# Kernel optimization log

Measured on AMD Instinct MI355X. Metric: run time of the kernel, lower is better.

The kernel has to match this reference:

```python
import jax, jax.numpy as jnp
import numpy as np

B, N, HID = 2, 512, 768
BIAF = 256
CLS = 14
CH = 32
SIZE_DIM = 25
N_POS = 30
HSZ = 2 * (BIAF + 1) + SIZE_DIM


def setup_inputs() -> dict:
    key = jax.random.key(0)
    ks = jax.random.split(key, 16)
    s = 0.02
    return {
        "x": jax.random.normal(ks[0], (B, N, HID), jnp.float32),
        "y": jax.random.normal(ks[1], (B, N, HID), jnp.float32),
        "z": jax.random.normal(ks[2], (B, N, N, CH), jnp.float32),
        "mlp1_w": jax.random.normal(ks[3], (BIAF, HID), jnp.float32) * s,
        "mlp1_b": jnp.zeros((BIAF,), jnp.float32),
        "mlp2_w": jax.random.normal(ks[4], (BIAF, HID), jnp.float32) * s,
        "mlp2_b": jnp.zeros((BIAF,), jnp.float32),
        "head_w": jax.random.normal(ks[5], (BIAF, HID), jnp.float32) * s,
        "head_b": jnp.zeros((BIAF,), jnp.float32),
        "tail_w": jax.random.normal(ks[6], (BIAF, HID), jnp.float32) * s,
        "tail_b": jnp.zeros((BIAF,), jnp.float32),
        "biaf_W": jax.random.normal(ks[7], (CLS, BIAF + 1, BIAF + 1), jnp.float32) * s,
        "W": jax.random.normal(ks[8], (CLS, HSZ), jnp.float32) * s,
        "size_emb": jax.random.normal(ks[9], (N_POS, SIZE_DIM), jnp.float32) * s,
    }


def reference(x, y, z, mlp1_w, mlp1_b, mlp2_w, mlp2_b, head_w, head_b,
              tail_w, tail_b, biaf_W, W, size_emb):
    # MLP branches (dropout=0 at eval; torch GELU is exact erf)
    h = jax.nn.gelu(x @ mlp1_w.T + mlp1_b, approximate=False)   # (b,m,BIAF)
    t = jax.nn.gelu(y @ mlp2_w.T + mlp2_b, approximate=False)   # (b,n,BIAF)
    ones = jnp.ones(h.shape[:-1] + (1,), h.dtype)
    h1 = jnp.concatenate([h, ones], -1)                          # (b,m,BIAF+1)
    t1 = jnp.concatenate([t, ones], -1)                          # (b,n,BIAF+1)
    # Biaffine with bias_x=bias_y=True -> (b,cls,m,n)
    o1 = jnp.einsum('bmi,kij,bnj->bkmn', h1, biaf_W, t1)

    # head/tail MLPs with LeakyReLU(0.01), then append 1-column
    head = jax.nn.leaky_relu(x @ head_w.T + head_b, 0.01)
    tail = jax.nn.leaky_relu(x @ tail_w.T + tail_b, 0.01)
    head = jnp.concatenate([head, ones], -1)                     # (b,m,BIAF+1)
    tail = jnp.concatenate([tail, ones], -1)                     # (b,n,BIAF+1)

    # einsum('bmnh,kh->bkmn', cat([head_m, tail_n, size_mn]), W) decomposed so
    # the (b,m,n,HSZ) pairwise tensor is never materialized (same math).
    d = head.shape[-1]
    Wh, Wt, Ws = W[:, :d], W[:, d:2 * d], W[:, 2 * d:]
    n = x.shape[1]
    ar = jnp.arange(n)
    ids = jnp.clip(ar[None, :] - ar[:, None], -N_POS // 2, N_POS // 2 - 1) + N_POS // 2
    se = size_emb[ids]                                           # (m,n,SIZE_DIM)
    o3 = (jnp.einsum('bmh,kh->bkm', head, Wh)[:, :, :, None]
          + jnp.einsum('bnh,kh->bkn', tail, Wt)[:, :, None, :]
          + jnp.einsum('mnh,kh->kmn', se, Ws)[None])
    return o1 + o3
```

## Files before the change

kernel.cpp:

```cpp
#include <hip/hip_runtime.h>
#include <hip/hip_bf16.h>
#include <math.h>
#include <stdint.h>

#define BDIM 2
#define NDIM 512
#define HID 768
#define BIAF 256
#define CLS 14
#define DD 257
#define NPOS 30
#define SDIM 25
#define HSZ 539
#define PK 288
#define PJ 384
#define ASTRIDE 296

typedef unsigned short ushort_t;
typedef __attribute__((ext_vector_type(8))) short short8;
typedef __attribute__((ext_vector_type(4))) float floatx4;
typedef __attribute__((ext_vector_type(4))) unsigned short ushort4_t;

#define MFMA16(a, b, c) __builtin_amdgcn_mfma_f32_16x16x32_bf16((a), (b), (c), 0, 0, 0)

__device__ inline float bf2f(ushort_t u) {
    union { unsigned int i; float f; } c; c.i = ((unsigned)u) << 16; return c.f;
}
__device__ inline ushort_t f2bf(float f) {
    __hip_bfloat16 h = __float2bfloat16(f);
    return *(ushort_t*)&h;
}

__device__ inline int xcd_swz(int bid, int nwg) {
    int q = nwg >> 3;
    return (bid & 7) * q + (bid >> 3);
}

__device__ inline void glds16(const ushort_t* g, const ushort_t* l) {
    __builtin_amdgcn_global_load_lds(
        (const __attribute__((address_space(1))) unsigned int*)(unsigned long long)(uintptr_t)g,
        (__attribute__((address_space(3))) unsigned int*)(unsigned int)(uintptr_t)l,
        16, 0, 0);
}


__global__ __launch_bounds__(256) void prep_all(
    const float* __restrict__ biafW, ushort_t* __restrict__ packW,
    const float* __restrict__ x, const float* __restrict__ y,
    const float* __restrict__ m1w, const float* __restrict__ m2w,
    const float* __restrict__ hw,  const float* __restrict__ tw,
    ushort_t* __restrict__ xhi, ushort_t* __restrict__ xlo,
    ushort_t* __restrict__ yhi, ushort_t* __restrict__ ylo,
    ushort_t* __restrict__ whi, ushort_t* __restrict__ wlo,
    ushort_t* __restrict__ h1hi, ushort_t* __restrict__ h1lo,
    ushort_t* __restrict__ t1hi, ushort_t* __restrict__ t1lo)
{
    const int bid = blockIdx.x;
    if (bid < 1512) {
        __shared__ float tile[32][33];
        const int ix = bid % 9;
        const int jy = (bid / 9) % 12;
        const int k  = bid / 108;
        const int i0 = ix * 32, j0 = jy * 32;
        const int r8 = threadIdx.x >> 5;
        const int c  = threadIdx.x & 31;
        #pragma unroll
        for (int rr = 0; rr < 4; ++rr) {
            int r = rr * 8 + r8;
            int gi = i0 + r, gj = j0 + c;
            tile[r][c] = (gi < DD && gj < DD) ? biafW[((size_t)k * DD + gi) * DD + gj] : 0.f;
        }
        __syncthreads();
        #pragma unroll
        for (int rr = 0; rr < 4; ++rr) {
            int jr = rr * 8 + r8;
            packW[((size_t)k * PJ + (j0 + jr)) * PK + i0 + c] = f2bf(tile[c][jr]);
        }
        return;
    }
    int tg = (bid - 1512) * 256 + threadIdx.x;
    if (tg < 196608) {
        int mat = tg / 49152;
        int e0  = (tg % 49152) * 4;
        const float* src = (mat == 0) ? m1w : (mat == 1) ? m2w : (mat == 2) ? hw : tw;
        float4 v = *(const float4*)(src + e0);
        size_t o = (size_t)mat * 196608 + e0;
        ushort4_t h, lo;
        h[0] = f2bf(v.x); lo[0] = f2bf(v.x - bf2f(h[0]));
        h[1] = f2bf(v.y); lo[1] = f2bf(v.y - bf2f(h[1]));
        h[2] = f2bf(v.z); lo[2] = f2bf(v.z - bf2f(h[2]));
        h[3] = f2bf(v.w); lo[3] = f2bf(v.w - bf2f(h[3]));
        *(ushort4_t*)(whi + o) = h;
        *(ushort4_t*)(wlo + o) = lo;
    } else if (tg < 589824) {
        int t = tg - 196608;
        int which = t / 196608;
        int e0 = (t % 196608) * 4;
        const float* src = which ? y : x;
        float4 v = *(const float4*)(src + e0);
        ushort4_t h, lo;
        h[0] = f2bf(v.x); lo[0] = f2bf(v.x - bf2f(h[0]));
        h[1] = f2bf(v.y); lo[1] = f2bf(v.y - bf2f(h[1]));
        h[2] = f2bf(v.z); lo[2] = f2bf(v.z - bf2f(h[2]));
        h[3] = f2bf(v.w); lo[3] = f2bf(v.w - bf2f(h[3]));
        *(ushort4_t*)((which ? yhi : xhi) + e0) = h;
        *(ushort4_t*)((which ? ylo : xlo) + e0) = lo;
    } else {
        int idx = tg - 589824;
        int plane = idx >> 15;
        int tok = (idx >> 5) & 1023;
        int c   = 256 + (idx & 31);
        ushort_t* dst = (plane == 0) ? h1hi : (plane == 1) ? h1lo : (plane == 2) ? t1hi : t1lo;
        ushort_t val = (c == 256 && (plane == 0 || plane == 2)) ? (ushort_t)0x3F80 : (ushort_t)0;
        dst[(size_t)tok * PK + c] = val;
    }
}

__global__ __launch_bounds__(256) void proj_mfma(
    const ushort_t* __restrict__ xhi, const ushort_t* __restrict__ xlo,
    const ushort_t* __restrict__ yhi, const ushort_t* __restrict__ ylo,
    const ushort_t* __restrict__ whi, const ushort_t* __restrict__ wlo,
    const float* __restrict__ m1b, const float* __restrict__ m2b,
    const float* __restrict__ hb,  const float* __restrict__ tb,
    ushort_t* __restrict__ h1hi, ushort_t* __restrict__ h1lo,
    ushort_t* __restrict__ t1hi, ushort_t* __restrict__ t1lo,
    float* __restrict__ headf, float* __restrict__ tailf)
{
    const int flat = xcd_swz(blockIdx.x, 512);
    const int ft = flat & 7;
    const int mt = (flat >> 3) & 15;
    const int proj = flat >> 7;
    const int wave = threadIdx.x >> 6, L = threadIdx.x & 63;
    const int quad = L >> 4, l16 = L & 15;
    const int tok0 = mt * 64 + wave * 16;
    const int f0 = ft * 32;

    const ushort_t* ahi_p = (proj == 1) ? yhi : xhi;
    const ushort_t* alo_p = (proj == 1) ? ylo : xlo;
    const float* bias = (proj == 0) ? m1b : (proj == 1) ? m2b : (proj == 2) ? hb : tb;

    const size_t aoff = (size_t)(tok0 + l16) * HID + quad * 8;
    const size_t wbase = (size_t)proj * BIAF * HID;
    const size_t b0 = wbase + (size_t)(f0 + l16) * HID + quad * 8;
    const size_t b1 = wbase + (size_t)(f0 + 16 + l16) * HID + quad * 8;

    floatx4 acc0 = {0.f, 0.f, 0.f, 0.f}, acc1 = {0.f, 0.f, 0.f, 0.f};
    #pragma unroll 4
    for (int k0 = 0; k0 < HID; k0 += 32) {
        short8 ah  = *(const short8*)(ahi_p + aoff + k0);
        short8 al  = *(const short8*)(alo_p + aoff + k0);
        short8 bh0 = *(const short8*)(whi + b0 + k0);
        short8 bl0 = *(const short8*)(wlo + b0 + k0);
        short8 bh1 = *(const short8*)(whi + b1 + k0);
        short8 bl1 = *(const short8*)(wlo + b1 + k0);
        acc0 = MFMA16(ah, bh0, acc0);
        acc1 = MFMA16(ah, bh1, acc1);
        acc0 = MFMA16(al, bh0, acc0);
        acc1 = MFMA16(al, bh1, acc1);
        acc0 = MFMA16(ah, bl0, acc0);
        acc1 = MFMA16(ah, bl1, acc1);
    }

    #pragma unroll
    for (int nf = 0; nf < 2; ++nf) {
        floatx4 a = nf ? acc1 : acc0;
        int feat = f0 + nf * 16 + l16;
        float bv = bias[feat];
        #pragma unroll
        for (int r = 0; r < 4; ++r) {
            int tok = tok0 + quad * 4 + r;
            float v = a[r] + bv;
            if (proj <= 1) {
                float g = 0.5f * v * (1.0f + erff(v * 0.70710678118654752f));
                ushort_t h = f2bf(g);
                ushort_t lo = f2bf(g - bf2f(h));
                if (proj == 0) { h1hi[(size_t)tok * PK + feat] = h; h1lo[(size_t)tok * PK + feat] = lo; }
                else           { t1hi[(size_t)tok * PK + feat] = h; t1lo[(size_t)tok * PK + feat] = lo; }
            } else {
                float lv = (v >= 0.f) ? v : 0.01f * v;
                if (proj == 2) headf[(size_t)tok * 256 + feat] = lv;
                else           tailf[(size_t)tok * 256 + feat] = lv;
            }
        }
    }
}

__global__ __launch_bounds__(256) void hk_tk_sk(
    const float* __restrict__ headf, const float* __restrict__ tailf,
    const float* __restrict__ W, const float* __restrict__ semb,
    float* __restrict__ hk, float* __restrict__ tk, float* __restrict__ skp)
{
    if (blockIdx.x >= 128) {
        int idx = (blockIdx.x - 128) * 256 + threadIdx.x;
        if (idx < CLS * NPOS) {
            int k = idx / NPOS, d = idx % NPOS;
            float acc = 0.f;
            for (int h = 0; h < SDIM; ++h)
                acc += semb[d*SDIM + h] * W[k*HSZ + 2*DD + h];
            skp[idx] = acc;
        }
        return;
    }
    int p = blockIdx.x * 256 + threadIdx.x;
    int which = p >> 14;
    int idx = p & 16383;
    int tok = idx >> 4;
    int k = idx & 15;
    if (k >= CLS) return;
    const float* row = (which ? tailf : headf) + (size_t)tok * 256;
    const float* wr = W + (size_t)k * HSZ + (which ? DD : 0);
    float acc = 0.f;
    for (int f4 = 0; f4 < 64; ++f4) {
        float4 rv = *(const float4*)(row + f4 * 4);
        acc += rv.x * wr[f4*4] + rv.y * wr[f4*4+1] + rv.z * wr[f4*4+2] + rv.w * wr[f4*4+3];
    }
    acc += wr[256];
    float* dst = which ? tk : hk;
    dst[(size_t)(tok >> 9) * CLS * NDIM + (size_t)k * NDIM + (tok & 511)] = acc;
}

__global__ __launch_bounds__(256) void biaf_fused(
    const ushort_t* __restrict__ h1hi, const ushort_t* __restrict__ h1lo,
    const ushort_t* __restrict__ packW,
    const ushort_t* __restrict__ t1hi, const ushort_t* __restrict__ t1lo,
    const float* __restrict__ hk, const float* __restrict__ tk,
    const float* __restrict__ sk,
    float* __restrict__ out)
{
    __shared__ __align__(16) ushort_t stage[16384];
    __shared__ __align__(16) ushort_t Aslab[32 * ASTRIDE];
    __shared__ float skr[NPOS];

    const int flat = xcd_swz(blockIdx.x, 448);
    const int mt = flat & 15, bk = flat >> 4;
    const int b = bk / CLS, k = bk % CLS;
    const int tid = threadIdx.x;
    if (tid < NPOS) skr[tid] = sk[k * NPOS + tid];
    const int wave = tid >> 6, L = tid & 63;
    const int quad = L >> 4, l16 = L & 15;
    const int sr = L >> 3, u = (L & 7) ^ sr;
    const int srow = 2 * sr + (u >> 2);
    const int scol = (u & 3) * 8;
    const int rbase = (l16 >> 1) * 64 + (((((l16 & 1) << 2) | quad) ^ (l16 >> 1)) * 8);
    const int m0 = mt * 32;

    const ushort_t* gAh = h1hi + (size_t)(b * NDIM + m0) * PK;
    const ushort_t* gAl = h1lo + (size_t)(b * NDIM + m0) * PK;
    const ushort_t* gB  = packW + (size_t)k * PJ * PK;

    const int mi = wave >> 1, jh = wave & 1;
    floatx4 accA[9];
    #pragma unroll
    for (int t = 0; t < 9; ++t)
        #pragma unroll
        for (int r = 0; r < 4; ++r) accA[t][r] = 0.f;

    for (int i0 = 0; i0 < PK; i0 += 32) {
        for (int s = wave; s < 22; s += 4) {
            const ushort_t* g; const ushort_t* l;
            if (s < 2)      { l = stage + s * 512;  g = gAh + (size_t)(s * 16 + srow) * PK + i0 + scol; }
            else if (s < 4) { l = stage + s * 512;  g = gAl + (size_t)((s - 2) * 16 + srow) * PK + i0 + scol; }
            else            { l = stage + s * 512;  g = gB  + (size_t)((s - 4) * 16 + srow) * PK + i0 + scol; }
            glds16(g, l);
        }
        __syncthreads();
        short8 ah = *(const short8*)(stage + mi * 512 + rbase);
        short8 al = *(const short8*)(stage + 1024 + mi * 512 + rbase);
        #pragma unroll
        for (int t = 0; t < 9; ++t) {
            short8 bt = *(const short8*)(stage + 2048 + (jh * 9 + t) * 512 + rbase);
            accA[t] = MFMA16(ah, bt, accA[t]);
            accA[t] = MFMA16(al, bt, accA[t]);
        }
        __syncthreads();
    }

    #pragma unroll
    for (int t = 0; t < 9; ++t) {
        int jb = (jh * 9 + t) * 16 + l16;
        #pragma unroll
        for (int r = 0; r < 4; ++r) {
            int row = mi * 16 + quad * 4 + r;
            Aslab[row * ASTRIDE + jb] = f2bf(accA[t][r]);
        }
    }
    __syncthreads();

    const int mi2 = wave >> 1, nh = wave & 1;
    const ushort_t* gTh = t1hi + (size_t)(b * NDIM) * PK;
    const ushort_t* gTl = t1lo + (size_t)(b * NDIM) * PK;

    auto stageB = [&](int bo, int nt, int js) {
        for (int s = wave; s < 16; s += 4) {
            const ushort_t* g; const ushort_t* l;
            if (s < 8) { l = stage + bo * 8192 + s * 512;
                         g = gTh + (size_t)(nt * 128 + s * 16 + srow) * PK + js * 32 + scol; }
            else       { l = stage + bo * 8192 + 4096 + (s - 8) * 512;
                         g = gTl + (size_t)(nt * 128 + (s - 8) * 16 + srow) * PK + js * 32 + scol; }
            glds16(g, l);
        }
    };

    stageB(0, 0, 0);
    __syncthreads();
    int cur = 0;
    const size_t obase = (size_t)bk * NDIM;

    for (int nt = 0; nt < 4; ++nt) {
        floatx4 accB[4];
        #pragma unroll
        for (int nf = 0; nf < 4; ++nf)
            #pragma unroll
            for (int r = 0; r < 4; ++r) accB[nf][r] = 0.f;

        for (int js = 0; js < 9; ++js) {
            int step = nt * 9 + js;
            if (step < 35) { int ns = step + 1; stageB(cur ^ 1, ns / 9, ns % 9); }
            short8 a = *(const short8*)(Aslab + (mi2 * 16 + l16) * ASTRIDE + js * 32 + quad * 8);
            #pragma unroll
            for (int nf = 0; nf < 4; ++nf) {
                short8 bh = *(const short8*)(stage + cur * 8192 + (nh * 4 + nf) * 512 + rbase);
                short8 bl = *(const short8*)(stage + cur * 8192 + 4096 + (nh * 4 + nf) * 512 + rbase);
                accB[nf] = MFMA16(a, bh, accB[nf]);
                accB[nf] = MFMA16(a, bl, accB[nf]);
            }
            __syncthreads();
            cur ^= 1;
        }

        int n0 = nt * 128;
        #pragma unroll
        for (int r = 0; r < 4; ++r) {
            int row = m0 + mi2 * 16 + quad * 4 + r;
            float hv = hk[obase + row];
            #pragma unroll
            for (int nf = 0; nf < 4; ++nf) {
                int col = n0 + nh * 64 + nf * 16 + l16;
                int d = col - row; d = d < -15 ? -15 : (d > 14 ? 14 : d); d += 15;
                out[(obase + row) * NDIM + col] = accB[nf][r] + hv + tk[obase + col] + skr[d];
            }
        }
    }
}

extern "C" void kernel_launch(void* const* d_in, const int* in_sizes, int n_in,
                              void* d_out, int out_size, void* d_ws, size_t ws_size,
                              hipStream_t stream) {
    const float* x    = (const float*)d_in[0];
    const float* y    = (const float*)d_in[1];
    const float* m1w  = (const float*)d_in[3];
    const float* m1b  = (const float*)d_in[4];
    const float* m2w  = (const float*)d_in[5];
    const float* m2b  = (const float*)d_in[6];
    const float* hw   = (const float*)d_in[7];
    const float* hb   = (const float*)d_in[8];
    const float* tw   = (const float*)d_in[9];
    const float* tb   = (const float*)d_in[10];
    const float* biafW= (const float*)d_in[11];
    const float* W    = (const float*)d_in[12];
    const float* semb = (const float*)d_in[13];

    char* p = (char*)d_ws;
    float* hk   = (float*)p;                    p += 57344;
    float* tk   = (float*)p;                    p += 57344;
    float* skp  = (float*)p;                    p += 2048;
    float* headf= (float*)p;                    p += 1048576;
    float* tailf= (float*)p;                    p += 1048576;
    ushort_t* h1hi = (ushort_t*)p;              p += 589824;
    ushort_t* h1lo = (ushort_t*)p;              p += 589824;
    ushort_t* t1hi = (ushort_t*)p;              p += 589824;
    ushort_t* t1lo = (ushort_t*)p;              p += 589824;
    ushort_t* packW= (ushort_t*)p;              p += 3096576;
    ushort_t* whi  = (ushort_t*)p;              p += 1572864;
    ushort_t* wlo  = (ushort_t*)p;              p += 1572864;
    ushort_t* xhi  = (ushort_t*)p;              p += 1572864;
    ushort_t* xlo  = (ushort_t*)p;              p += 1572864;
    ushort_t* yhi  = (ushort_t*)p;              p += 1572864;
    ushort_t* ylo  = (ushort_t*)p;              p += 1572864;

    prep_all<<<4328, 256, 0, stream>>>(biafW, packW, x, y, m1w, m2w, hw, tw,
                                       xhi, xlo, yhi, ylo, whi, wlo,
                                       h1hi, h1lo, t1hi, t1lo);
    proj_mfma<<<512, 256, 0, stream>>>(xhi, xlo, yhi, ylo, whi, wlo,
                                       m1b, m2b, hb, tb,
                                       h1hi, h1lo, t1hi, t1lo, headf, tailf);
    hk_tk_sk<<<130, 256, 0, stream>>>(headf, tailf, W, semb, hk, tk, skp);
    biaf_fused<<<448, 256, 0, stream>>>(h1hi, h1lo, packW, t1hi, t1lo,
                                        hk, tk, skp, (float*)d_out);
}
```

Baseline: 207.5 us.

## Pre-tile operands into MFMA fragment layout and load directly from global

Operands h1/t1 and the packed biaffine weight are now stored in 16x32 fragment-tiled order, so each lane reads its short8 MFMA fragment straight from global memory. This removes the LDS staging buffer, the global_load_lds double-buffering and the per-step barriers in the biaffine kernel. The packed weight also drops its padding from 384 to 288 rows. The grid doubles by splitting the output columns in half, with an occupancy hint of 4 blocks. The trade-off is that stage 1 is recomputed in both halves, and reads now go through cache without explicit prefetching or overlap.

```diff
diff --git a/kernel.cpp b/kernel.cpp
--- a/kernel.cpp
+++ b/kernel.cpp
@@ -13,8 +13,8 @@
 #define SDIM 25
 #define HSZ 539
 #define PK 288
-#define PJ 384
 #define ASTRIDE 296
+
 
 typedef unsigned short ushort_t;
 typedef __attribute__((ext_vector_type(8))) short short8;
@@ -35,14 +35,6 @@
     int q = nwg >> 3;
     return (bid & 7) * q + (bid >> 3);
 }
-
-__device__ inline void glds16(const ushort_t* g, const ushort_t* l) {
-    __builtin_amdgcn_global_load_lds(
-        (const __attribute__((address_space(1))) unsigned int*)(unsigned long long)(uintptr_t)g,
-        (__attribute__((address_space(3))) unsigned int*)(unsigned int)(uintptr_t)l,
-        16, 0, 0);
-}
-
 
 __global__ __launch_bounds__(256) void prep_all(
     const float* __restrict__ biafW, ushort_t* __restrict__ packW,
@@ -56,11 +48,11 @@
     ushort_t* __restrict__ t1hi, ushort_t* __restrict__ t1lo)
 {
     const int bid = blockIdx.x;
-    if (bid < 1512) {
+    if (bid < 1134) {
         __shared__ float tile[32][33];
         const int ix = bid % 9;
-        const int jy = (bid / 9) % 12;
-        const int k  = bid / 108;
+        const int jy = (bid / 9) % 9;
+        const int k  = bid / 81;
         const int i0 = ix * 32, j0 = jy * 32;
         const int r8 = threadIdx.x >> 5;
         const int c  = threadIdx.x & 31;
@@ -74,11 +66,13 @@
         #pragma unroll
         for (int rr = 0; rr < 4; ++rr) {
             int jr = rr * 8 + r8;
-            packW[((size_t)k * PJ + (j0 + jr)) * PK + i0 + c] = f2bf(tile[c][jr]);
+            int j = j0 + jr;
+            size_t addr = ((size_t)(k * 18 + (j >> 4)) * 9 + ix) * 512 + (j & 15) * 32 + c;
+            packW[addr] = f2bf(tile[c][jr]);
         }
         return;
     }
-    int tg = (bid - 1512) * 256 + threadIdx.x;
+    int tg = (bid - 1134) * 256 + threadIdx.x;
     if (tg < 196608) {
         int mat = tg / 49152;
         int e0  = (tg % 49152) * 4;
@@ -109,10 +103,11 @@
         int idx = tg - 589824;
         int plane = idx >> 15;
         int tok = (idx >> 5) & 1023;
-        int c   = 256 + (idx & 31);
+        int c   = idx & 31;
+        int bb = tok >> 9, m = tok & 511;
         ushort_t* dst = (plane == 0) ? h1hi : (plane == 1) ? h1lo : (plane == 2) ? t1hi : t1lo;
-        ushort_t val = (c == 256 && (plane == 0 || plane == 2)) ? (ushort_t)0x3F80 : (ushort_t)0;
-        dst[(size_t)tok * PK + c] = val;
+        ushort_t val = (c == 0 && (plane == 0 || plane == 2)) ? (ushort_t)0x3F80 : (ushort_t)0;
+        dst[((size_t)(bb * 32 + (m >> 4)) * 9 + 8) * 512 + (m & 15) * 32 + c] = val;
     }
 }
 
@@ -174,8 +169,11 @@
                 float g = 0.5f * v * (1.0f + erff(v * 0.70710678118654752f));
                 ushort_t h = f2bf(g);
                 ushort_t lo = f2bf(g - bf2f(h));
-                if (proj == 0) { h1hi[(size_t)tok * PK + feat] = h; h1lo[(size_t)tok * PK + feat] = lo; }
-                else           { t1hi[(size_t)tok * PK + feat] = h; t1lo[(size_t)tok * PK + feat] = lo; }
+                int bb = tok >> 9, m = tok & 511;
+                size_t ad = ((size_t)(bb * 32 + (m >> 4)) * 9 + (feat >> 5)) * 512
+                          + (m & 15) * 32 + (feat & 31);
+                if (proj == 0) { h1hi[ad] = h; h1lo[ad] = lo; }
+                else           { t1hi[ad] = h; t1lo[ad] = lo; }
             } else {
                 float lv = (v >= 0.f) ? v : 0.01f * v;
                 if (proj == 2) headf[(size_t)tok * 256 + feat] = lv;
@@ -219,7 +217,7 @@
     dst[(size_t)(tok >> 9) * CLS * NDIM + (size_t)k * NDIM + (tok & 511)] = acc;
 }
 
-__global__ __launch_bounds__(256) void biaf_fused(
+__global__ __launch_bounds__(256, 4) void biaf_fused(
     const ushort_t* __restrict__ h1hi, const ushort_t* __restrict__ h1lo,
     const ushort_t* __restrict__ packW,
     const ushort_t* __restrict__ t1hi, const ushort_t* __restrict__ t1lo,
@@ -227,52 +225,40 @@
     const float* __restrict__ sk,
     float* __restrict__ out)
 {
-    __shared__ __align__(16) ushort_t stage[16384];
     __shared__ __align__(16) ushort_t Aslab[32 * ASTRIDE];
     __shared__ float skr[NPOS];
 
-    const int flat = xcd_swz(blockIdx.x, 448);
-    const int mt = flat & 15, bk = flat >> 4;
+    const int flat = xcd_swz(blockIdx.x, 896);
+    const int ns = flat & 1, mt = (flat >> 1) & 15, bk = flat >> 5;
     const int b = bk / CLS, k = bk % CLS;
     const int tid = threadIdx.x;
     if (tid < NPOS) skr[tid] = sk[k * NPOS + tid];
     const int wave = tid >> 6, L = tid & 63;
     const int quad = L >> 4, l16 = L & 15;
-    const int sr = L >> 3, u = (L & 7) ^ sr;
-    const int srow = 2 * sr + (u >> 2);
-    const int scol = (u & 3) * 8;
-    const int rbase = (l16 >> 1) * 64 + (((((l16 & 1) << 2) | quad) ^ (l16 >> 1)) * 8);
+    const int frag = l16 * 32 + quad * 8;
     const int m0 = mt * 32;
 
-    const ushort_t* gAh = h1hi + (size_t)(b * NDIM + m0) * PK;
-    const ushort_t* gAl = h1lo + (size_t)(b * NDIM + m0) * PK;
-    const ushort_t* gB  = packW + (size_t)k * PJ * PK;
-
     const int mi = wave >> 1, jh = wave & 1;
+    const ushort_t* Ah_t = h1hi + (size_t)((b * 32 + mt * 2 + mi) * 9) * 512;
+    const ushort_t* Al_t = h1lo + (size_t)((b * 32 + mt * 2 + mi) * 9) * 512;
+    const ushort_t* Wp   = packW + (size_t)k * 18 * 9 * 512;
+
     floatx4 accA[9];
     #pragma unroll
     for (int t = 0; t < 9; ++t)
         #pragma unroll
         for (int r = 0; r < 4; ++r) accA[t][r] = 0.f;
 
-    for (int i0 = 0; i0 < PK; i0 += 32) {
-        for (int s = wave; s < 22; s += 4) {
-            const ushort_t* g; const ushort_t* l;
-            if (s < 2)      { l = stage + s * 512;  g = gAh + (size_t)(s * 16 + srow) * PK + i0 + scol; }
-            else if (s < 4) { l = stage + s * 512;  g = gAl + (size_t)((s - 2) * 16 + srow) * PK + i0 + scol; }
-            else            { l = stage + s * 512;  g = gB  + (size_t)((s - 4) * 16 + srow) * PK + i0 + scol; }
-            glds16(g, l);
-        }
-        __syncthreads();
-        short8 ah = *(const short8*)(stage + mi * 512 + rbase);
-        short8 al = *(const short8*)(stage + 1024 + mi * 512 + rbase);
+    #pragma unroll 3
+    for (int it = 0; it < 9; ++it) {
+        short8 ah = *(const short8*)(Ah_t + it * 512 + frag);
+        short8 al = *(const short8*)(Al_t + it * 512 + frag);
         #pragma unroll
         for (int t = 0; t < 9; ++t) {
-            short8 bt = *(const short8*)(stage + 2048 + (jh * 9 + t) * 512 + rbase);
+            short8 bt = *(const short8*)(Wp + (size_t)((jh * 9 + t) * 9 + it) * 512 + frag);
             accA[t] = MFMA16(ah, bt, accA[t]);
             accA[t] = MFMA16(al, bt, accA[t]);
         }
-        __syncthreads();
     }
 
     #pragma unroll
@@ -287,45 +273,28 @@
     __syncthreads();
 
     const int mi2 = wave >> 1, nh = wave & 1;
-    const ushort_t* gTh = t1hi + (size_t)(b * NDIM) * PK;
-    const ushort_t* gTl = t1lo + (size_t)(b * NDIM) * PK;
-
-    auto stageB = [&](int bo, int nt, int js) {
-        for (int s = wave; s < 16; s += 4) {
-            const ushort_t* g; const ushort_t* l;
-            if (s < 8) { l = stage + bo * 8192 + s * 512;
-                         g = gTh + (size_t)(nt * 128 + s * 16 + srow) * PK + js * 32 + scol; }
-            else       { l = stage + bo * 8192 + 4096 + (s - 8) * 512;
-                         g = gTl + (size_t)(nt * 128 + (s - 8) * 16 + srow) * PK + js * 32 + scol; }
-            glds16(g, l);
-        }
-    };
-
-    stageB(0, 0, 0);
-    __syncthreads();
-    int cur = 0;
+    const size_t tb0 = (size_t)(b * 32) * 9 * 512;
     const size_t obase = (size_t)bk * NDIM;
 
-    for (int nt = 0; nt < 4; ++nt) {
+    for (int ntl = 0; ntl < 2; ++ntl) {
+        const int nt = ns * 2 + ntl;
         floatx4 accB[4];
         #pragma unroll
         for (int nf = 0; nf < 4; ++nf)
             #pragma unroll
             for (int r = 0; r < 4; ++r) accB[nf][r] = 0.f;
 
+        #pragma unroll 3
         for (int js = 0; js < 9; ++js) {
-            int step = nt * 9 + js;
-            if (step < 35) { int ns = step + 1; stageB(cur ^ 1, ns / 9, ns % 9); }
             short8 a = *(const short8*)(Aslab + (mi2 * 16 + l16) * ASTRIDE + js * 32 + quad * 8);
             #pragma unroll
             for (int nf = 0; nf < 4; ++nf) {
-                short8 bh = *(const short8*)(stage + cur * 8192 + (nh * 4 + nf) * 512 + rbase);
-                short8 bl = *(const short8*)(stage + cur * 8192 + 4096 + (nh * 4 + nf) * 512 + rbase);
+                const size_t toff = tb0 + (size_t)((nt * 8 + nh * 4 + nf) * 9 + js) * 512 + frag;
+                short8 bh = *(const short8*)(t1hi + toff);
+                short8 bl = *(const short8*)(t1lo + toff);
                 accB[nf] = MFMA16(a, bh, accB[nf]);
                 accB[nf] = MFMA16(a, bl, accB[nf]);
             }
-            __syncthreads();
-            cur ^= 1;
         }
 
         int n0 = nt * 128;
@@ -370,7 +339,7 @@
     ushort_t* h1lo = (ushort_t*)p;              p += 589824;
     ushort_t* t1hi = (ushort_t*)p;              p += 589824;
     ushort_t* t1lo = (ushort_t*)p;              p += 589824;
-    ushort_t* packW= (ushort_t*)p;              p += 3096576;
+    ushort_t* packW= (ushort_t*)p;              p += 2322432;
     ushort_t* whi  = (ushort_t*)p;              p += 1572864;
     ushort_t* wlo  = (ushort_t*)p;              p += 1572864;
     ushort_t* xhi  = (ushort_t*)p;              p += 1572864;
@@ -378,13 +347,13 @@
     ushort_t* yhi  = (ushort_t*)p;              p += 1572864;
     ushort_t* ylo  = (ushort_t*)p;              p += 1572864;
 
-    prep_all<<<4328, 256, 0, stream>>>(biafW, packW, x, y, m1w, m2w, hw, tw,
+    prep_all<<<3950, 256, 0, stream>>>(biafW, packW, x, y, m1w, m2w, hw, tw,
                                        xhi, xlo, yhi, ylo, whi, wlo,
                                        h1hi, h1lo, t1hi, t1lo);
     proj_mfma<<<512, 256, 0, stream>>>(xhi, xlo, yhi, ylo, whi, wlo,
                                        m1b, m2b, hb, tb,
                                        h1hi, h1lo, t1hi, t1lo, headf, tailf);
     hk_tk_sk<<<130, 256, 0, stream>>>(headf, tailf, W, semb, hk, tk, skp);
-    biaf_fused<<<448, 256, 0, stream>>>(h1hi, h1lo, packW, t1hi, t1lo,
+    biaf_fused<<<896, 256, 0, stream>>>(h1hi, h1lo, packW, t1hi, t1lo,
                                         hk, tk, skp, (float*)d_out);
 }
```

After: 232.4 us. +12.0%, slower.
